# Performance work log

Measured on AMD Instinct MI355X. Metric: run time of the kernel, lower is better.

The kernel has to match this reference:

```python
import jax, jax.numpy as jnp
import numpy as np

G = 128          # voxel grid extent per axis
N = 400_000      # number of occupied voxels
K = 27           # 3^3 kernel offsets


def _build_kernel_maps(rng):
    # Sample N unique occupied voxels in a G^3 grid.
    flat = rng.choice(G ** 3, size=N, replace=False).astype(np.int64)
    z = flat % G
    y = (flat // G) % G
    x = flat // (G * G)
    order = np.argsort(flat)
    keys = flat[order]  # sorted flat coords, keys[i] belongs to voxel order[i]

    in_idx = np.full((K, N), N, dtype=np.int32)   # pad with dummy index N
    out_idx = np.full((K, N), N, dtype=np.int32)
    k = 0
    for dx in (-1, 0, 1):
        for dy in (-1, 0, 1):
            for dz in (-1, 0, 1):
                nx, ny, nz = x + dx, y + dy, z + dz
                valid = ((nx >= 0) & (nx < G) & (ny >= 0) & (ny < G)
                         & (nz >= 0) & (nz < G))
                nflat = nx * G * G + ny * G + nz
                vidx = np.nonzero(valid)[0]
                pos = np.searchsorted(keys, nflat[vidx])
                pos_cl = np.clip(pos, 0, N - 1)
                hit = keys[pos_cl] == nflat[vidx]
                src = order[pos_cl[hit]].astype(np.int32)  # neighbor voxel (input)
                dst = vidx[hit].astype(np.int32)           # center voxel (output)
                in_idx[k, : src.shape[0]] = src
                out_idx[k, : dst.shape[0]] = dst
                k += 1
    return in_idx, out_idx


def setup_inputs() -> dict:
    rng = np.random.default_rng(0)
    in_idx, out_idx = _build_kernel_maps(rng)
    key = jax.random.key(0)
    k1, k2, k3 = jax.random.split(key, 3)
    feat = jax.random.normal(k1, (N, 128), dtype=jnp.float32)
    # kaiming-like scale: std = sqrt(2 / fan_out)
    kernel1 = jax.random.normal(k2, (K, 128, 14), dtype=jnp.float32) * np.sqrt(2.0 / 14)
    kernel2 = jax.random.normal(k3, (K, 14, 14), dtype=jnp.float32) * np.sqrt(2.0 / 14)
    return {"feat": feat, "kernel1": kernel1, "kernel2": kernel2,
            "in_idx": jnp.asarray(in_idx), "out_idx": jnp.asarray(out_idx)}


def _sparse_conv(feat, kernel, in_idx, out_idx):
    # gather -> GEMM -> scatter-add per kernel offset (MinkowskiConvolution, bias=False)
    n = feat.shape[0]
    fp = jnp.concatenate([feat, jnp.zeros((1, feat.shape[1]), feat.dtype)], axis=0)
    out = jnp.zeros((n + 1, kernel.shape[2]), feat.dtype)
    for k in range(kernel.shape[0]):
        out = out.at[out_idx[k]].add(fp[in_idx[k]] @ kernel[k])
    return out[:n]


def reference(feat, kernel1, kernel2, in_idx, out_idx):
    x = _sparse_conv(feat, kernel1, in_idx, out_idx)
    x = jax.nn.gelu(x, approximate=False)  # MinkowskiGELU == exact torch GELU
    x = _sparse_conv(x, kernel2, in_idx, out_idx)
    return x
```

## Files before the change

kernel.cpp:

```cpp
#include <hip/hip_runtime.h>
#include <math.h>

#define NK 27
#define C1 128
#define C2 14
#define X1S 16
#define PROW 16
#define CAP 131072
#define WIN 4096

__global__ __launch_bounds__(256) void ranges_kernel(
    const int* __restrict__ out_idx, int* __restrict__ r, int N, int nwin)
{
    int t = blockIdx.x * 256 + threadIdx.x;
    int total = NK * (nwin + 1);
    if (t >= total) return;
    int mm = t / (nwin + 1);
    int b  = t % (nwin + 1);
    long tgt_l = (long)b * WIN; if (tgt_l > N) tgt_l = N;
    int target = (int)tgt_l;
    const int* a = out_idx + (size_t)mm * N;
    int lo = 0, hi = N;
    while (lo < hi) { int mid = (lo + hi) >> 1; if (a[mid] < target) lo = mid + 1; else hi = mid; }
    r[t] = lo;
}

__global__ __launch_bounds__(256) void pslot_kernel(
    const int* __restrict__ in_idx, int* __restrict__ pslot, int N)
{
    const int mm = blockIdx.x;
    const int j0 = blockIdx.y * 256;
    const int* src = in_idx + (size_t)mm * N;
    if (src[j0] >= N) return;
    int j = j0 + threadIdx.x;
    if (j >= N) return;
    int v = src[j];
    if (v >= N) return;
    if (mm != 13 && j >= CAP) return;
    int base = (mm == 13) ? 0 : N + ((mm < 13) ? mm : mm - 1) * CAP;
    pslot[(size_t)v * 28 + mm] = base + j;
}


__global__ __launch_bounds__(256) void conv1A_kernel(
    const float* __restrict__ feat, const float* __restrict__ W1,
    const int* __restrict__ out_idx, const int* __restrict__ r,
    float* __restrict__ P, int N, int nwin)
{
    int lin  = blockIdx.x;
    int xcd  = lin & 7;
    int slot = lin >> 3;
    int mm   = slot % NK;
    int b    = (slot / NK) * 8 + xcd;
    if (b >= nwin) return;

    int jlo = r[mm * (nwin + 1) + b];
    int jhi = r[mm * (nwin + 1) + b + 1];
    if (mm != 13 && jhi > CAP) jhi = CAP;
    if (jlo >= jhi) return;

    __shared__ float Wl[C2 * C1];
    const int k = 26 - mm;
    const int tid = threadIdx.x;
    for (int t = tid; t < C2 * C1; t += 256) {
        int c = t >> 7, i = t & 127;
        Wl[t] = W1[k * (C1 * C2) + i * C2 + c];
    }
    __syncthreads();

    const int base = (mm == 13) ? 0 : N + ((mm < 13) ? mm : mm - 1) * CAP;
    const int* gidx = out_idx + (size_t)mm * N;

    for (int j0 = jlo + tid; j0 < jhi; j0 += 1024) {
        int  jj[4];
        bool val[4];
        #pragma unroll
        for (int p = 0; p < 4; ++p) {
            int j = j0 + p * 256;
            val[p] = (j < jhi);
            jj[p]  = val[p] ? j : (jhi - 1);
        }
        const float4* f0 = (const float4*)(feat + (size_t)gidx[jj[0]] * C1);
        const float4* f1 = (const float4*)(feat + (size_t)gidx[jj[1]] * C1);
        const float4* f2 = (const float4*)(feat + (size_t)gidx[jj[2]] * C1);
        const float4* f3 = (const float4*)(feat + (size_t)gidx[jj[3]] * C1);

        float acc[4][C2];
        #pragma unroll
        for (int p = 0; p < 4; ++p)
            #pragma unroll
            for (int c = 0; c < C2; ++c) acc[p][c] = 0.f;

        #pragma unroll 2
        for (int i4 = 0; i4 < C1 / 4; ++i4) {
            float4 a0 = f0[i4], a1 = f1[i4], a2 = f2[i4], a3 = f3[i4];
            #pragma unroll
            for (int c = 0; c < C2; ++c) {
                float4 w = *(const float4*)&Wl[c * C1 + i4 * 4];
                acc[0][c] = fmaf(a0.x, w.x, fmaf(a0.y, w.y, fmaf(a0.z, w.z, fmaf(a0.w, w.w, acc[0][c]))));
                acc[1][c] = fmaf(a1.x, w.x, fmaf(a1.y, w.y, fmaf(a1.z, w.z, fmaf(a1.w, w.w, acc[1][c]))));
                acc[2][c] = fmaf(a2.x, w.x, fmaf(a2.y, w.y, fmaf(a2.z, w.z, fmaf(a2.w, w.w, acc[2][c]))));
                acc[3][c] = fmaf(a3.x, w.x, fmaf(a3.y, w.y, fmaf(a3.z, w.z, fmaf(a3.w, w.w, acc[3][c]))));
            }
        }

        #pragma unroll
        for (int p = 0; p < 4; ++p) {
            if (!val[p]) continue;
            float* pp = P + (size_t)(base + jj[p]) * PROW;
            *(float4*)(pp + 0)  = make_float4(acc[p][0],  acc[p][1],  acc[p][2],  acc[p][3]);
            *(float4*)(pp + 4)  = make_float4(acc[p][4],  acc[p][5],  acc[p][6],  acc[p][7]);
            *(float4*)(pp + 8)  = make_float4(acc[p][8],  acc[p][9],  acc[p][10], acc[p][11]);
            *(float4*)(pp + 12) = make_float4(acc[p][12], acc[p][13], 0.f, 0.f);
        }
    }
}

__global__ __launch_bounds__(256) void conv1B_kernel(
    const float* __restrict__ P, const int* __restrict__ pslot,
    float* __restrict__ x1, int N)
{
    int v = blockIdx.x * 256 + threadIdx.x;
    if (v >= N) return;
    const int4* ps = (const int4*)(pslot + (size_t)v * 28);
    int s[28];
    #pragma unroll
    for (int q = 0; q < 7; ++q) {
        int4 t = ps[q];
        s[q * 4 + 0] = t.x; s[q * 4 + 1] = t.y; s[q * 4 + 2] = t.z; s[q * 4 + 3] = t.w;
    }
    float acc[C2];
    #pragma unroll
    for (int c = 0; c < C2; ++c) acc[c] = 0.f;
    #pragma unroll
    for (int mm = 0; mm < NK; ++mm) {
        int sl = s[mm];
        if (sl < 0) continue;
        const float4* q = (const float4*)(P + (size_t)sl * PROW);
        float4 a = q[0], b = q[1], c4 = q[2], d = q[3];
        acc[0] += a.x;  acc[1] += a.y;  acc[2] += a.z;  acc[3] += a.w;
        acc[4] += b.x;  acc[5] += b.y;  acc[6] += b.z;  acc[7] += b.w;
        acc[8] += c4.x; acc[9] += c4.y; acc[10] += c4.z; acc[11] += c4.w;
        acc[12] += d.x; acc[13] += d.y;
    }
    #pragma unroll
    for (int c = 0; c < C2; ++c) {
        float x = acc[c];
        acc[c] = 0.5f * x * (1.0f + erff(x * 0.70710678118654752f));
    }
    float* o = x1 + (size_t)v * X1S;
    *(float4*)(o + 0)  = make_float4(acc[0], acc[1], acc[2], acc[3]);
    *(float4*)(o + 4)  = make_float4(acc[4], acc[5], acc[6], acc[7]);
    *(float4*)(o + 8)  = make_float4(acc[8], acc[9], acc[10], acc[11]);
    *(float4*)(o + 12) = make_float4(acc[12], acc[13], 0.f, 0.f);
}

__global__ __launch_bounds__(256) void conv2A_kernel(
    const float* __restrict__ x1, const float* __restrict__ W2,
    const int* __restrict__ out_idx, const int* __restrict__ r,
    float* __restrict__ P, int N, int nwin)
{
    int lin  = blockIdx.x;
    int xcd  = lin & 7;
    int slot = lin >> 3;
    int mm   = slot % NK;
    int b    = (slot / NK) * 8 + xcd;
    if (b >= nwin) return;

    int jlo = r[mm * (nwin + 1) + b];
    int jhi = r[mm * (nwin + 1) + b + 1];
    if (mm != 13 && jhi > CAP) jhi = CAP;
    if (jlo >= jhi) return;

    __shared__ float Wl[C2 * 16];
    const int k = 26 - mm;
    const int tid = threadIdx.x;
    if (tid < C2 * C2) {
        int c = tid / C2, i = tid % C2;
        Wl[c * 16 + i] = W2[k * (C2 * C2) + i * C2 + c];
    }
    __syncthreads();

    const int base = (mm == 13) ? 0 : N + ((mm < 13) ? mm : mm - 1) * CAP;
    const int* gidx = out_idx + (size_t)mm * N;

    for (int j0 = jlo + tid; j0 < jhi; j0 += 512) {
        int  jj[2];
        bool val[2];
        #pragma unroll
        for (int p = 0; p < 2; ++p) {
            int j = j0 + p * 256;
            val[p] = (j < jhi);
            jj[p]  = val[p] ? j : (jhi - 1);
        }
        float f[2][C2];
        #pragma unroll
        for (int p = 0; p < 2; ++p) {
            const float* rrow = x1 + (size_t)gidx[jj[p]] * X1S;
            float4 q0 = *(const float4*)(rrow + 0);
            float4 q1 = *(const float4*)(rrow + 4);
            float4 q2 = *(const float4*)(rrow + 8);
            float2 q3 = *(const float2*)(rrow + 12);
            f[p][0] = q0.x; f[p][1] = q0.y; f[p][2]  = q0.z; f[p][3]  = q0.w;
            f[p][4] = q1.x; f[p][5] = q1.y; f[p][6]  = q1.z; f[p][7]  = q1.w;
            f[p][8] = q2.x; f[p][9] = q2.y; f[p][10] = q2.z; f[p][11] = q2.w;
            f[p][12] = q3.x; f[p][13] = q3.y;
        }
        float acc[2][C2];
        #pragma unroll
        for (int c = 0; c < C2; ++c) {
            float s0 = 0.f, s1 = 0.f;
            #pragma unroll
            for (int i = 0; i < C2; ++i) {
                float w = Wl[c * 16 + i];
                s0 = fmaf(f[0][i], w, s0);
                s1 = fmaf(f[1][i], w, s1);
            }
            acc[0][c] = s0;
            acc[1][c] = s1;
        }
        #pragma unroll
        for (int p = 0; p < 2; ++p) {
            if (!val[p]) continue;
            float* pp = P + (size_t)(base + jj[p]) * PROW;
            *(float4*)(pp + 0)  = make_float4(acc[p][0],  acc[p][1],  acc[p][2],  acc[p][3]);
            *(float4*)(pp + 4)  = make_float4(acc[p][4],  acc[p][5],  acc[p][6],  acc[p][7]);
            *(float4*)(pp + 8)  = make_float4(acc[p][8],  acc[p][9],  acc[p][10], acc[p][11]);
            *(float4*)(pp + 12) = make_float4(acc[p][12], acc[p][13], 0.f, 0.f);
        }
    }
}

__global__ __launch_bounds__(256) void conv2B_kernel(
    const float* __restrict__ P, const int* __restrict__ pslot,
    float* __restrict__ out, int N)
{
    int v = blockIdx.x * 256 + threadIdx.x;
    if (v >= N) return;
    const int4* ps = (const int4*)(pslot + (size_t)v * 28);
    int s[28];
    #pragma unroll
    for (int q = 0; q < 7; ++q) {
        int4 t = ps[q];
        s[q * 4 + 0] = t.x; s[q * 4 + 1] = t.y; s[q * 4 + 2] = t.z; s[q * 4 + 3] = t.w;
    }
    float acc[C2];
    #pragma unroll
    for (int c = 0; c < C2; ++c) acc[c] = 0.f;
    #pragma unroll
    for (int mm = 0; mm < NK; ++mm) {
        int sl = s[mm];
        if (sl < 0) continue;
        const float4* q = (const float4*)(P + (size_t)sl * PROW);
        float4 a = q[0], b = q[1], c4 = q[2], d = q[3];
        acc[0] += a.x;  acc[1] += a.y;  acc[2] += a.z;  acc[3] += a.w;
        acc[4] += b.x;  acc[5] += b.y;  acc[6] += b.z;  acc[7] += b.w;
        acc[8] += c4.x; acc[9] += c4.y; acc[10] += c4.z; acc[11] += c4.w;
        acc[12] += d.x; acc[13] += d.y;
    }
    float* o = out + (size_t)v * C2;
    *(float2*)(o + 0)  = make_float2(acc[0], acc[1]);
    *(float2*)(o + 2)  = make_float2(acc[2], acc[3]);
    *(float2*)(o + 4)  = make_float2(acc[4], acc[5]);
    *(float2*)(o + 6)  = make_float2(acc[6], acc[7]);
    *(float2*)(o + 8)  = make_float2(acc[8], acc[9]);
    *(float2*)(o + 10) = make_float2(acc[10], acc[11]);
    *(float2*)(o + 12) = make_float2(acc[12], acc[13]);
}

__global__ __launch_bounds__(256) void fb_conv1_kernel(
    const float* __restrict__ feat, const float* __restrict__ W1,
    const int* __restrict__ in_idx, const int* __restrict__ out_idx,
    float* __restrict__ x1, int N)
{
    __shared__ float Wl[C2 * C1];
    const int k = blockIdx.y;
    const int tid = threadIdx.x;
    for (int t = tid; t < C2 * C1; t += 256) {
        int c = t >> 7, i = t & 127;
        Wl[t] = W1[k * (C1 * C2) + i * C2 + c];
    }
    __syncthreads();
    const int jbase = (blockIdx.x * 256 + tid) * 4;
    if (jbase >= N) return;
    int src[4], dst[4];
    for (int p = 0; p < 4; ++p) {
        int j = jbase + p;
        src[p] = (j < N) ? in_idx[(size_t)k * N + j]  : N;
        dst[p] = (j < N) ? out_idx[(size_t)k * N + j] : N;
    }
    bool valid[4]; bool any = false;
    for (int p = 0; p < 4; ++p) { valid[p] = (dst[p] < N); any |= valid[p]; if (!valid[p]) src[p] = 0; }
    if (!any) return;
    float acc[4][C2];
    for (int p = 0; p < 4; ++p) for (int c = 0; c < C2; ++c) acc[p][c] = 0.f;
    for (int i4 = 0; i4 < C1 / 4; ++i4) {
        float4 a = ((const float4*)(feat + (size_t)src[0] * C1))[i4];
        float4 b = ((const float4*)(feat + (size_t)src[1] * C1))[i4];
        float4 cc = ((const float4*)(feat + (size_t)src[2] * C1))[i4];
        float4 d = ((const float4*)(feat + (size_t)src[3] * C1))[i4];
        for (int c = 0; c < C2; ++c) {
            float4 w = *(const float4*)&Wl[c * C1 + i4 * 4];
            acc[0][c] = fmaf(a.x, w.x, fmaf(a.y, w.y, fmaf(a.z, w.z, fmaf(a.w, w.w, acc[0][c]))));
            acc[1][c] = fmaf(b.x, w.x, fmaf(b.y, w.y, fmaf(b.z, w.z, fmaf(b.w, w.w, acc[1][c]))));
            acc[2][c] = fmaf(cc.x, w.x, fmaf(cc.y, w.y, fmaf(cc.z, w.z, fmaf(cc.w, w.w, acc[2][c]))));
            acc[3][c] = fmaf(d.x, w.x, fmaf(d.y, w.y, fmaf(d.z, w.z, fmaf(d.w, w.w, acc[3][c]))));
        }
    }
    for (int p = 0; p < 4; ++p) {
        if (!valid[p]) continue;
        float* o = x1 + (size_t)dst[p] * X1S;
        for (int c = 0; c < C2; ++c) atomicAdd(o + c, acc[p][c]);
    }
}

__global__ __launch_bounds__(256) void fb_gelu_kernel(float* __restrict__ x, int total4)
{
    int i = blockIdx.x * 256 + threadIdx.x;
    if (i >= total4) return;
    float4 v = ((float4*)x)[i];
    v.x = 0.5f * v.x * (1.0f + erff(v.x * 0.70710678118654752f));
    v.y = 0.5f * v.y * (1.0f + erff(v.y * 0.70710678118654752f));
    v.z = 0.5f * v.z * (1.0f + erff(v.z * 0.70710678118654752f));
    v.w = 0.5f * v.w * (1.0f + erff(v.w * 0.70710678118654752f));
    ((float4*)x)[i] = v;
}

__global__ __launch_bounds__(256) void fb_conv2_kernel(
    const float* __restrict__ x1, const float* __restrict__ W2,
    const int* __restrict__ in_idx, const int* __restrict__ out_idx,
    float* __restrict__ out, int N)
{
    __shared__ float Wl[C2 * 16];
    const int k = blockIdx.y;
    const int tid = threadIdx.x;
    if (tid < C2 * C2) {
        int c = tid / C2, i = tid % C2;
        Wl[c * 16 + i] = W2[k * (C2 * C2) + i * C2 + c];
    }
    __syncthreads();
    const int j = blockIdx.x * 256 + tid;
    if (j >= N) return;
    int src = in_idx[(size_t)k * N + j];
    int dst = out_idx[(size_t)k * N + j];
    if (dst >= N) return;
    const float* rrow = x1 + (size_t)src * X1S;
    float f[C2];
    for (int i = 0; i < C2; ++i) f[i] = rrow[i];
    float* o = out + (size_t)dst * C2;
    for (int c = 0; c < C2; ++c) {
        float sum = 0.f;
        for (int i = 0; i < C2; ++i) sum = fmaf(f[i], Wl[c * 16 + i], sum);
        atomicAdd(o + c, sum);
    }
}

extern "C" void kernel_launch(void* const* d_in, const int* in_sizes, int n_in,
                              void* d_out, int out_size, void* d_ws, size_t ws_size,
                              hipStream_t stream)
{
    const float* feat    = (const float*)d_in[0];
    const float* W1      = (const float*)d_in[1];
    const float* W2      = (const float*)d_in[2];
    const int*   in_idx  = (const int*)d_in[3];
    const int*   out_idx = (const int*)d_in[4];
    float*       out     = (float*)d_out;

    const int N    = in_sizes[0] / C1;
    const int nwin = (N + WIN - 1) / WIN;

    const size_t prows      = (size_t)N + 26ull * CAP;
    const size_t p_bytes    = prows * PROW * sizeof(float);
    const size_t pslot_bytes = (size_t)N * 28 * sizeof(int);
    const size_t x1_bytes   = (size_t)N * X1S * sizeof(float);
    const size_t r_bytes    = (size_t)NK * (nwin + 1) * sizeof(int);
    const size_t need = p_bytes + pslot_bytes + x1_bytes + ((r_bytes + 255) & ~255ull) + 1024;

    if (ws_size >= need) {
        char* w = (char*)d_ws;
        float* P     = (float*)w;                 w += p_bytes;
        int*   pslot = (int*)w;                   w += pslot_bytes;
        float* x1    = (float*)w;                 w += x1_bytes;
        int*   r     = (int*)w;

        hipMemsetAsync(pslot, 0xFF, pslot_bytes, stream);

        int rtot = NK * (nwin + 1);
        ranges_kernel<<<(rtot + 255) / 256, 256, 0, stream>>>(out_idx, r, N, nwin);

        {
            dim3 grid(NK, (N + 255) / 256);
            pslot_kernel<<<grid, 256, 0, stream>>>(in_idx, pslot, N);
        }
        const int nb = 8 * ((nwin + 7) / 8) * NK;
        conv1A_kernel<<<nb, 256, 0, stream>>>(feat, W1, out_idx, r, P, N, nwin);
        conv1B_kernel<<<(N + 255) / 256, 256, 0, stream>>>(P, pslot, x1, N);
        conv2A_kernel<<<nb, 256, 0, stream>>>(x1, W2, out_idx, r, P, N, nwin);
        conv2B_kernel<<<(N + 255) / 256, 256, 0, stream>>>(P, pslot, out, N);
    } else {
        float* x1 = (float*)d_ws;
        hipMemsetAsync(x1, 0, x1_bytes, stream);
        hipMemsetAsync(out, 0, (size_t)out_size * sizeof(float), stream);
        {
            dim3 grid((N + 1023) / 1024, NK);
            fb_conv1_kernel<<<grid, 256, 0, stream>>>(feat, W1, in_idx, out_idx, x1, N);
        }
        {
            int total4 = N * X1S / 4;
            fb_gelu_kernel<<<(total4 + 255) / 256, 256, 0, stream>>>(x1, total4);
        }
        {
            dim3 grid((N + 255) / 256, NK);
            fb_conv2_kernel<<<grid, 256, 0, stream>>>(x1, W2, in_idx, out_idx, out, N);
        }
    }
}
```

Measured before the change: 891.8 us.

## Enlarge output windows and split identity offset into four direct chunks

Raises the output window size so each block covers a larger contiguous output range per offset. The identity offset (mm=13), which is dense, gets four separate chunk blocks per region and skips the index gather by using the row index directly. It also sets a 3-blocks-per-CU launch bound, deepens the conv1 inner unroll, and widens conv2A to four rows per thread using full float4 loads. These aim to balance load across blocks and cut index-load overhead, at the cost of fewer blocks for the sparse offsets and possible register pressure.

```diff
diff --git a/kernel.cpp b/kernel.cpp
--- a/kernel.cpp
+++ b/kernel.cpp
@@ -7,16 +7,17 @@
 #define X1S 16
 #define PROW 16
 #define CAP 131072
-#define WIN 4096
+#define WIN 16704
+#define CHID (WIN/4)
 
 __global__ __launch_bounds__(256) void ranges_kernel(
-    const int* __restrict__ out_idx, int* __restrict__ r, int N, int nwin)
+    const int* __restrict__ out_idx, int* __restrict__ r, int N, int nreg)
 {
     int t = blockIdx.x * 256 + threadIdx.x;
-    int total = NK * (nwin + 1);
+    int total = NK * (nreg + 1);
     if (t >= total) return;
-    int mm = t / (nwin + 1);
-    int b  = t % (nwin + 1);
+    int mm = t / (nreg + 1);
+    int b  = t % (nreg + 1);
     long tgt_l = (long)b * WIN; if (tgt_l > N) tgt_l = N;
     int target = (int)tgt_l;
     const int* a = out_idx + (size_t)mm * N;
@@ -42,29 +43,41 @@
 }
 
 
-__global__ __launch_bounds__(256) void conv1A_kernel(
+__global__ __launch_bounds__(256, 3) void conv1A_kernel(
     const float* __restrict__ feat, const float* __restrict__ W1,
     const int* __restrict__ out_idx, const int* __restrict__ r,
-    float* __restrict__ P, int N, int nwin)
-{
-    int lin  = blockIdx.x;
-    int xcd  = lin & 7;
-    int slot = lin >> 3;
-    int mm   = slot % NK;
-    int b    = (slot / NK) * 8 + xcd;
-    if (b >= nwin) return;
-
-    int jlo = r[mm * (nwin + 1) + b];
-    int jhi = r[mm * (nwin + 1) + b + 1];
-    if (mm != 13 && jhi > CAP) jhi = CAP;
-    if (jlo >= jhi) return;
+    float* __restrict__ P, int N, int nreg)
+{
+    int lin = blockIdx.x;
+    int xcd = lin & 7;
+    int t   = lin >> 3;
+    int s   = t % 30;
+    int rg8 = t / 30;
+    int reg = rg8 * 8 + xcd;
+    if (reg >= nreg) return;
+
+    int mm, jlo, jhi;
+    const bool ident = (s >= 26);
+    if (ident) {
+        mm = 13;
+        int c = reg * 4 + (s - 26);
+        jlo = c * CHID;
+        if (jlo >= N) return;
+        jhi = jlo + CHID; if (jhi > N) jhi = N;
+    } else {
+        mm = s + (s >= 13);
+        jlo = r[mm * (nreg + 1) + reg];
+        jhi = r[mm * (nreg + 1) + reg + 1];
+        if (jhi > CAP) jhi = CAP;
+        if (jlo >= jhi) return;
+    }
 
     __shared__ float Wl[C2 * C1];
     const int k = 26 - mm;
     const int tid = threadIdx.x;
-    for (int t = tid; t < C2 * C1; t += 256) {
-        int c = t >> 7, i = t & 127;
-        Wl[t] = W1[k * (C1 * C2) + i * C2 + c];
+    for (int tt = tid; tt < C2 * C1; tt += 256) {
+        int c = tt >> 7, i = tt & 127;
+        Wl[tt] = W1[k * (C1 * C2) + i * C2 + c];
     }
     __syncthreads();
 
@@ -74,16 +87,24 @@
     for (int j0 = jlo + tid; j0 < jhi; j0 += 1024) {
         int  jj[4];
         bool val[4];
+        int  vv[4];
         #pragma unroll
         for (int p = 0; p < 4; ++p) {
             int j = j0 + p * 256;
             val[p] = (j < jhi);
             jj[p]  = val[p] ? j : (jhi - 1);
         }
-        const float4* f0 = (const float4*)(feat + (size_t)gidx[jj[0]] * C1);
-        const float4* f1 = (const float4*)(feat + (size_t)gidx[jj[1]] * C1);
-        const float4* f2 = (const float4*)(feat + (size_t)gidx[jj[2]] * C1);
-        const float4* f3 = (const float4*)(feat + (size_t)gidx[jj[3]] * C1);
+        if (ident) {
+            #pragma unroll
+            for (int p = 0; p < 4; ++p) vv[p] = jj[p];
+        } else {
+            #pragma unroll
+            for (int p = 0; p < 4; ++p) vv[p] = gidx[jj[p]];
+        }
+        const float4* f0 = (const float4*)(feat + (size_t)vv[0] * C1);
+        const float4* f1 = (const float4*)(feat + (size_t)vv[1] * C1);
+        const float4* f2 = (const float4*)(feat + (size_t)vv[2] * C1);
+        const float4* f3 = (const float4*)(feat + (size_t)vv[3] * C1);
 
         float acc[4][C2];
         #pragma unroll
@@ -91,7 +112,7 @@
             #pragma unroll
             for (int c = 0; c < C2; ++c) acc[p][c] = 0.f;
 
-        #pragma unroll 2
+        #pragma unroll 4
         for (int i4 = 0; i4 < C1 / 4; ++i4) {
             float4 a0 = f0[i4], a1 = f1[i4], a2 = f2[i4], a3 = f3[i4];
             #pragma unroll
@@ -155,22 +176,34 @@
     *(float4*)(o + 12) = make_float4(acc[12], acc[13], 0.f, 0.f);
 }
 
-__global__ __launch_bounds__(256) void conv2A_kernel(
+__global__ __launch_bounds__(256, 3) void conv2A_kernel(
     const float* __restrict__ x1, const float* __restrict__ W2,
     const int* __restrict__ out_idx, const int* __restrict__ r,
-    float* __restrict__ P, int N, int nwin)
-{
-    int lin  = blockIdx.x;
-    int xcd  = lin & 7;
-    int slot = lin >> 3;
-    int mm   = slot % NK;
-    int b    = (slot / NK) * 8 + xcd;
-    if (b >= nwin) return;
-
-    int jlo = r[mm * (nwin + 1) + b];
-    int jhi = r[mm * (nwin + 1) + b + 1];
-    if (mm != 13 && jhi > CAP) jhi = CAP;
-    if (jlo >= jhi) return;
+    float* __restrict__ P, int N, int nreg)
+{
+    int lin = blockIdx.x;
+    int xcd = lin & 7;
+    int t   = lin >> 3;
+    int s   = t % 30;
+    int rg8 = t / 30;
+    int reg = rg8 * 8 + xcd;
+    if (reg >= nreg) return;
+
+    int mm, jlo, jhi;
+    const bool ident = (s >= 26);
+    if (ident) {
+        mm = 13;
+        int c = reg * 4 + (s - 26);
+        jlo = c * CHID;
+        if (jlo >= N) return;
+        jhi = jlo + CHID; if (jhi > N) jhi = N;
+    } else {
+        mm = s + (s >= 13);
+        jlo = r[mm * (nreg + 1) + reg];
+        jhi = r[mm * (nreg + 1) + reg + 1];
+        if (jhi > CAP) jhi = CAP;
+        if (jlo >= jhi) return;
+    }
 
     __shared__ float Wl[C2 * 16];
     const int k = 26 - mm;
@@ -184,43 +217,49 @@
     const int base = (mm == 13) ? 0 : N + ((mm < 13) ? mm : mm - 1) * CAP;
     const int* gidx = out_idx + (size_t)mm * N;
 
-    for (int j0 = jlo + tid; j0 < jhi; j0 += 512) {
-        int  jj[2];
-        bool val[2];
-        #pragma unroll
-        for (int p = 0; p < 2; ++p) {
+    for (int j0 = jlo + tid; j0 < jhi; j0 += 1024) {
+        int  jj[4];
+        bool val[4];
+        int  vv[4];
+        #pragma unroll
+        for (int p = 0; p < 4; ++p) {
             int j = j0 + p * 256;
             val[p] = (j < jhi);
             jj[p]  = val[p] ? j : (jhi - 1);
         }
-        float f[2][C2];
-        #pragma unroll
-        for (int p = 0; p < 2; ++p) {
-            const float* rrow = x1 + (size_t)gidx[jj[p]] * X1S;
-            float4 q0 = *(const float4*)(rrow + 0);
-            float4 q1 = *(const float4*)(rrow + 4);
-            float4 q2 = *(const float4*)(rrow + 8);
-            float2 q3 = *(const float2*)(rrow + 12);
+        if (ident) {
+            #pragma unroll
+            for (int p = 0; p < 4; ++p) vv[p] = jj[p];
+        } else {
+            #pragma unroll
+            for (int p = 0; p < 4; ++p) vv[p] = gidx[jj[p]];
+        }
+        float f[4][C2 + 2];
+        #pragma unroll
+        for (int p = 0; p < 4; ++p) {
+            const float4* rrow = (const float4*)(x1 + (size_t)vv[p] * X1S);
+            float4 q0 = rrow[0], q1 = rrow[1], q2 = rrow[2], q3 = rrow[3];
             f[p][0] = q0.x; f[p][1] = q0.y; f[p][2]  = q0.z; f[p][3]  = q0.w;
             f[p][4] = q1.x; f[p][5] = q1.y; f[p][6]  = q1.z; f[p][7]  = q1.w;
             f[p][8] = q2.x; f[p][9] = q2.y; f[p][10] = q2.z; f[p][11] = q2.w;
             f[p][12] = q3.x; f[p][13] = q3.y;
         }
-        float acc[2][C2];
+        float acc[4][C2];
         #pragma unroll
         for (int c = 0; c < C2; ++c) {
-            float s0 = 0.f, s1 = 0.f;
+            float s0 = 0.f, s1 = 0.f, s2 = 0.f, s3 = 0.f;
             #pragma unroll
             for (int i = 0; i < C2; ++i) {
                 float w = Wl[c * 16 + i];
                 s0 = fmaf(f[0][i], w, s0);
                 s1 = fmaf(f[1][i], w, s1);
+                s2 = fmaf(f[2][i], w, s2);
+                s3 = fmaf(f[3][i], w, s3);
             }
-            acc[0][c] = s0;
-            acc[1][c] = s1;
-        }
-        #pragma unroll
-        for (int p = 0; p < 2; ++p) {
+            acc[0][c] = s0; acc[1][c] = s1; acc[2][c] = s2; acc[3][c] = s3;
+        }
+        #pragma unroll
+        for (int p = 0; p < 4; ++p) {
             if (!val[p]) continue;
             float* pp = P + (size_t)(base + jj[p]) * PROW;
             *(float4*)(pp + 0)  = make_float4(acc[p][0],  acc[p][1],  acc[p][2],  acc[p][3]);
@@ -367,13 +406,13 @@
     float*       out     = (float*)d_out;
 
     const int N    = in_sizes[0] / C1;
-    const int nwin = (N + WIN - 1) / WIN;
+    const int nreg = (N + WIN - 1) / WIN;
 
     const size_t prows      = (size_t)N + 26ull * CAP;
     const size_t p_bytes    = prows * PROW * sizeof(float);
     const size_t pslot_bytes = (size_t)N * 28 * sizeof(int);
     const size_t x1_bytes   = (size_t)N * X1S * sizeof(float);
-    const size_t r_bytes    = (size_t)NK * (nwin + 1) * sizeof(int);
+    const size_t r_bytes    = (size_t)NK * (nreg + 1) * sizeof(int);
     const size_t need = p_bytes + pslot_bytes + x1_bytes + ((r_bytes + 255) & ~255ull) + 1024;
 
     if (ws_size >= need) {
@@ -385,17 +424,17 @@
 
         hipMemsetAsync(pslot, 0xFF, pslot_bytes, stream);
 
-        int rtot = NK * (nwin + 1);
-        ranges_kernel<<<(rtot + 255) / 256, 256, 0, stream>>>(out_idx, r, N, nwin);
+        int rtot = NK * (nreg + 1);
+        ranges_kernel<<<(rtot + 255) / 256, 256, 0, stream>>>(out_idx, r, N, nreg);
 
         {
             dim3 grid(NK, (N + 255) / 256);
             pslot_kernel<<<grid, 256, 0, stream>>>(in_idx, pslot, N);
         }
-        const int nb = 8 * ((nwin + 7) / 8) * NK;
-        conv1A_kernel<<<nb, 256, 0, stream>>>(feat, W1, out_idx, r, P, N, nwin);
+        const int nb = 8 * ((nreg + 7) / 8) * 30;
+        conv1A_kernel<<<nb, 256, 0, stream>>>(feat, W1, out_idx, r, P, N, nreg);
         conv1B_kernel<<<(N + 255) / 256, 256, 0, stream>>>(P, pslot, x1, N);
-        conv2A_kernel<<<nb, 256, 0, stream>>>(x1, W2, out_idx, r, P, N, nwin);
+        conv2A_kernel<<<nb, 256, 0, stream>>>(x1, W2, out_idx, r, P, N, nreg);
         conv2B_kernel<<<(N + 255) / 256, 256, 0, stream>>>(P, pslot, out, N);
     } else {
         float* x1 = (float*)d_ws;
```

New measurement: 1.152 ms. 29.2% more time.
